# Kernel tuning notes

Measured on AMD Instinct MI355X. Metric: run time of the kernel, lower is better.

The kernel has to match this reference:

```python
import jax, jax.numpy as jnp
import numpy as np

G = 16          # graphs per side
NPG = 512       # nodes per graph
NSIDE = G * NPG # 8192 nodes per side
N = 2 * NSIDE   # 16384 nodes in combined batched graph
EPG = 4096      # edges per graph
E = 2 * G * EPG # 131072 edges
IN = 64; HID = 64; NH = 8; NC = 3
ALPHA = 0.2; EPS = 1e-5


def setup_inputs() -> dict:
    key = jax.random.key(0)
    ks = jax.random.split(key, 20)
    s = 0.05
    off = jnp.repeat(jnp.arange(2 * G, dtype=jnp.int32) * NPG, EPG)
    return {
        'nbd1': jax.random.normal(ks[0], (NSIDE, IN), jnp.float32),
        'nbd2': jax.random.normal(ks[1], (NSIDE, IN), jnp.float32),
        'ebd': jax.random.normal(ks[2], (E, IN), jnp.float32),
        'src': jax.random.randint(ks[3], (E,), 0, NPG, jnp.int32) + off,
        'dst': jax.random.randint(ks[4], (E,), 0, NPG, jnp.int32) + off,
        'node_gid': jnp.repeat(jnp.arange(2 * G, dtype=jnp.int32), NPG),
        'projW': jax.random.normal(ks[5], (4 * IN, HID), jnp.float32) * s,
        'W1': jax.random.normal(ks[6], (IN, NH * HID), jnp.float32) * s,
        'al1': jax.random.normal(ks[7], (NH, HID), jnp.float32) * s,
        'ar1': jax.random.normal(ks[8], (NH, HID), jnp.float32) * s,
        'ae1': jax.random.normal(ks[9], (NH, HID), jnp.float32) * s,
        'W2': jax.random.normal(ks[10], (NH * HID, NH * HID), jnp.float32) * s,
        'al2': jax.random.normal(ks[11], (NH, HID), jnp.float32) * s,
        'ar2': jax.random.normal(ks[12], (NH, HID), jnp.float32) * s,
        'ae2': jax.random.normal(ks[13], (NH, HID), jnp.float32) * s,
        'bn1_g': jnp.ones((2 * NH * HID,), jnp.float32),
        'bn1_b': jnp.zeros((2 * NH * HID,), jnp.float32),
        'fc1_W': jax.random.normal(ks[14], (2 * NH * HID, HID), jnp.float32) * s,
        'fc1_b': jnp.zeros((HID,), jnp.float32),
        'bn2_g': jnp.ones((HID,), jnp.float32),
        'bn2_b': jnp.zeros((HID,), jnp.float32),
        'fc2_W': jax.random.normal(ks[15], (HID, NC), jnp.float32) * s,
        'fc2_b': jnp.zeros((NC,), jnp.float32),
    }


def _segment_softmax(s, seg, n):
    # s: [E, H]; softmax over edges sharing the same destination node
    m = jax.ops.segment_max(s, seg, num_segments=n)
    ex = jnp.exp(s - m[seg])
    z = jax.ops.segment_sum(ex, seg, num_segments=n)
    return ex / jnp.maximum(z[seg], 1e-9)


def _gat_layer(hn, he, src, dst, n, W, al, ar, ae):
    nh, d = al.shape
    ft = (hn @ W).reshape(n, nh, d)            # [N,H,D]
    eft = (he @ W).reshape(-1, nh, d)          # [E,H,D]
    a1 = jnp.einsum('nhd,hd->nh', ft, al)
    a2 = jnp.einsum('nhd,hd->nh', ft, ar)
    a3 = jnp.einsum('ehd,hd->eh', eft, ae)
    a = a1[src] + a3 + a2[dst]                 # [E,H]
    a = jnp.where(a > 0, a, ALPHA * a)         # LeakyReLU(0.2)
    alpha = _segment_softmax(a, dst, n)[:, :, None]  # [E,H,1]
    f_cat = eft * alpha + ft[src] * alpha      # weighted edge + weighted src feat
    nft = jax.ops.segment_sum(f_cat, dst, num_segments=n)
    ret1 = jax.nn.elu(nft.reshape(n, nh * d))
    ret2 = jax.nn.elu(f_cat.reshape(f_cat.shape[0], nh * d))
    return ret1, ret2


def _bn(x, g, b):
    mu = jnp.mean(x, axis=0)
    v = jnp.var(x, axis=0)
    return (x - mu) * jax.lax.rsqrt(v + EPS) * g + b


def _forward(nbd1, nbd2, ebd, src, dst, node_gid, projW,
             W1, al1, ar1, ae1, W2, al2, ar2, ae2,
             bn1_g, bn1_b, fc1_W, fc1_b, bn2_g, bn2_b, fc2_W, fc2_b):
    # Node alignment (cross-graph soft attention, 2-D tensors as in source)
    att = nbd1 @ nbd2.T                                   # [N1,N2]
    x1a = jax.nn.softmax(att, axis=-1) @ nbd2
    x2a = jax.nn.softmax(att.T, axis=-1) @ nbd1
    q1 = jnp.concatenate([nbd1, x1a, nbd1 - x1a, nbd1 * x1a], axis=-1)
    q2 = jnp.concatenate([nbd2, x2a, nbd2 - x2a, nbd2 * x2a], axis=-1)
    h1 = jax.nn.relu(q1 @ projW)
    h2 = jax.nn.relu(q2 @ projW)
    h_n = jnp.concatenate([h1, h2], axis=0)               # [N,HID]
    h_e = ebd
    h_n, h_e = _gat_layer(h_n, h_e, src, dst, N, W1, al1, ar1, ae1)
    h_n, h_e = _gat_layer(h_n, h_e, src, dst, N, W2, al2, ar2, ae2)
    # dgl.mean_nodes
    cnt = jax.ops.segment_sum(jnp.ones((N,), h_n.dtype), node_gid, num_segments=2 * G)
    hg = jax.ops.segment_sum(h_n, node_gid, num_segments=2 * G) / cnt[:, None]
    x = jnp.concatenate([hg[:G], hg[G:2 * G]], axis=1)    # [G, 2*NH*HID]
    x = _bn(x, bn1_g, bn1_b)
    x = jax.nn.relu(x @ fc1_W + fc1_b)
    x = _bn(x, bn2_g, bn2_b)
    return x @ fc2_W + fc2_b                              # [G, NC]


def reference(nbd1, nbd2, ebd, src, dst, node_gid, projW,
              W1, al1, ar1, ae1, W2, al2, ar2, ae2,
              bn1_g, bn1_b, fc1_W, fc1_b, bn2_g, bn2_b, fc2_W, fc2_b):
    return _forward(nbd1, nbd2, ebd, src, dst, node_gid, projW,
                    W1, al1, ar1, ae1, W2, al2, ar2, ae2,
                    bn1_g, bn1_b, fc1_W, fc1_b, bn2_g, bn2_b, fc2_W, fc2_b)
```

## Files before the change

kernel.cpp:

```cpp
#include <hip/hip_runtime.h>


#define NSd 8192
#define NNd 16384
#define NEd 131072
#define KSPLIT 8

typedef unsigned short u16;
typedef unsigned int   u32;
typedef short bf16x8 __attribute__((ext_vector_type(8)));
typedef float f32x4  __attribute__((ext_vector_type(4)));
typedef float f32x16 __attribute__((ext_vector_type(16)));

__device__ __forceinline__ float bf2f(u16 u){ return __uint_as_float(((u32)u) << 16); }
__device__ __forceinline__ u16 f2bf(float f){
  u32 u = __float_as_uint(f);
  u += 0x7fffu + ((u >> 16) & 1u);
  return (u16)(u >> 16);
}
__device__ __forceinline__ u32 pkbf(float a, float b){
  u32 r;
  asm("v_cvt_pk_bf16_f32 %0, %1, %2" : "=v"(r) : "v"(a), "v"(b));
  return r;
}
__device__ __forceinline__ void pl32swap(u32& a, u32& b){
  auto r = __builtin_amdgcn_permlane32_swap(a, b, false, false);
  a = r[0]; b = r[1];
}
__device__ __forceinline__ float eluf(float x){ return x > 0.f ? x : expm1f(x); }
__device__ __forceinline__ float leaky(float x){ return x > 0.f ? x : 0.2f * x; }
__device__ __forceinline__ float ldin(const void* p, size_t i, int fl){
  return fl ? bf2f(((const u16*)p)[i]) : ((const float*)p)[i];
}
__device__ __forceinline__ void lse_merge(float& m, float& z, float om, float oz){
  float M = fmaxf(m, om);
  z = z * __expf(m - M) + oz * __expf(om - M);
  m = M;
}

static constexpr size_t OFF_WF   = 0;
static constexpr size_t OFF_CB   = 1529600;
static constexpr size_t OFF_U    = 1584896;
static constexpr size_t OFF_W1B  = 18362112;
static constexpr size_t OFF_W2B  = 18427648;
static constexpr size_t OFF_WE2B = 18951936;
static constexpr size_t OFF_AL1  = 35139328;
static constexpr size_t OFF_SA   = 39333632;
static constexpr size_t OFF_HNA  = 43527936;
static constexpr size_t OFF_DEG  = 77082368;
static constexpr size_t OFF_RP   = 77147904;
static constexpr size_t OFF_FILL = 77213696;
static constexpr size_t OFF_CIDX = 77279232;
static constexpr size_t OFF_RBIG = 77803520;
static constexpr size_t OFF_T    = 111357952;
static constexpr size_t OFF_XCAT = 144912384;
static constexpr size_t OFF_FLAG = 144977920;
static constexpr size_t WS_NEED  = 144978176;

static constexpr size_t T_X1A = 0;
static constexpr size_t T_X2A = 2097152;
static constexpr size_t T_HN0 = 4194304;
static constexpr size_t T_PZ  = 4194304;
static constexpr size_t T_AN1 = 8388608;
static constexpr size_t T_S   = 9437184;
static constexpr size_t T_Y   = 0;
static constexpr size_t T_G2  = 16777216;
static constexpr size_t T_Y1G = 0;
static constexpr size_t R_AN2 = 17301504;

static constexpr int WO_PROJ = 0,      WO_W1 = 16384;
static constexpr int WO_AL1 = 49152,   WO_AR1 = 49664,  WO_AE1 = 50176;
static constexpr int WO_W2  = 50688;
static constexpr int WO_AL2 = 312832,  WO_AR2 = 313344, WO_AE2 = 313856;
static constexpr int WO_B1G = 314368,  WO_B1B = 315392;
static constexpr int WO_F1W = 316416,  WO_F1B = 381952;
static constexpr int WO_B2G = 382016,  WO_B2B = 382080;
static constexpr int WO_F2W = 382144,  WO_F2B = 382336;
static constexpr int WO_END = 382339;

static constexpr int CB_WC1 = 0;
static constexpr int CB_WE1 = 1024;
static constexpr int CB_WC2 = 1536;
static constexpr int CB_WE2 = 9728;
static constexpr int CB_END = 13824;

__global__ __launch_bounds__(256) void detect_k(const u16* __restrict__ p, int* __restrict__ flag){
  __shared__ int bad;
  if (threadIdx.x == 0) bad = 0;
  __syncthreads();
  int b = 0;
  for (int i = threadIdx.x; i < 1024; i += 256){
    float f = bf2f(p[i]);
    if (!(fabsf(f) <= 100.f)) b++;
  }
  atomicAdd(&bad, b);
  __syncthreads();
  if (threadIdx.x == 0) *flag = (bad == 0) ? 1 : 0;
}

struct P17 { const void* p[17]; };

__global__ __launch_bounds__(256) void convw_k(P17 ps, float* __restrict__ wf, const int* __restrict__ flagp){
  const int i = blockIdx.x * 256 + threadIdx.x;
  if (i >= WO_END) return;
  const int fl = *flagp;
  const int ends[17] = {16384,49152,49664,50176,50688,312832,313344,313856,314368,
                        315392,316416,381952,382016,382080,382144,382336,382339};
  int seg = 0;
  while (i >= ends[seg]) seg++;
  const int start = seg ? ends[seg-1] : 0;
  wf[i] = ldin(ps.p[seg], i - start, fl);
}

__global__ __launch_bounds__(256) void convwT_k(const float* __restrict__ wf, u16* __restrict__ w1t,
                                                u16* __restrict__ w2t){
  const int i = blockIdx.x * 256 + threadIdx.x;
  if (i < 32768){
    const int c = i >> 6, k = i & 63;
    w1t[i] = f2bf(wf[WO_W1 + k * 512 + c]);
  } else if (i < 32768 + 262144){
    const int j = i - 32768;
    const int c = j >> 9, k = j & 511;
    w2t[j] = f2bf(wf[WO_W2 + k * 512 + c]);
  }
}

__global__ __launch_bounds__(256) void combos_k(const float* __restrict__ wf, float* __restrict__ cb,
                                                u16* __restrict__ we2b){
  const int i = blockIdx.x * 256 + threadIdx.x;
  if (i >= CB_END + 4096) return;
  if (i >= CB_END){ we2b[4096 + (i - CB_END)] = 0; return; }
  float acc = 0.f;
  if (i < 1024){
    const int o = i >> 6, d = i & 63, h = o & 7;
    const float* a = wf + ((o >> 3) ? WO_AR1 : WO_AL1) + h * 64;
    for (int dp = 0; dp < 64; dp++) acc += wf[WO_W1 + d * 512 + h * 64 + dp] * a[dp];
    cb[CB_WC1 + i] = acc;
  } else if (i < 1536){
    const int j = i - 1024, h = j >> 6, d = j & 63;
    for (int dp = 0; dp < 64; dp++) acc += wf[WO_W1 + d * 512 + h * 64 + dp] * wf[WO_AE1 + h * 64 + dp];
    cb[CB_WE1 + j] = acc;
  } else if (i < 9728){
    const int j = i - 1536, o = j >> 9, c = j & 511, h = o & 7;
    for (int dp = 0; dp < 64; dp++){
      const float av = (o >> 3) ? wf[WO_AR2 + h * 64 + dp]
                                : (wf[WO_AL2 + h * 64 + dp] - wf[WO_AE2 + h * 64 + dp]);
      acc += wf[WO_W2 + c * 512 + h * 64 + dp] * av;
    }
    cb[CB_WC2 + j] = acc;
  } else {
    const int j = i - 9728, h = j >> 9, c = j & 511;
    for (int dp = 0; dp < 64; dp++) acc += wf[WO_W2 + c * 512 + h * 64 + dp] * wf[WO_AE2 + h * 64 + dp];
    cb[CB_WE2 + j] = acc;
    we2b[j] = f2bf(acc);
  }
}

__global__ __launch_bounds__(256) void flash_mfma_k(const void* __restrict__ Qp, const void* __restrict__ Kp,
                                                    const int* __restrict__ flagp, float* __restrict__ pacc,
                                                    float* __restrict__ pz){
  const int fl = *flagp;
  __shared__ __align__(16) u16 Ks[2][32][64];
  __shared__ __align__(16) u16 Kt[2][64][40];
  const int t = threadIdx.x;
  const int w = t >> 6, l = t & 63;
  const int hi = l >> 5, ql = l & 31;
  const int q0 = blockIdx.x * 128;
  const int kbeg = blockIdx.y * 1024;
  const int sr = t & 31, scg = t >> 5;
  const int kp = t & 15, dq = t >> 4;

  bf16x8 bq[4];
  {
    const int qrow = q0 + w * 32 + ql;
    if (fl){
      const u16* qp = (const u16*)Qp + (size_t)qrow * 64 + hi * 8;
      #pragma unroll
      for (int s = 0; s < 4; s++) bq[s] = *(const bf16x8*)(qp + s * 16);
    } else {
      const float* qp = (const float*)Qp + (size_t)qrow * 64 + hi * 8;
      #pragma unroll
      for (int s = 0; s < 4; s++){
        union { u32 w_[4]; bf16x8 v; } u;
        #pragma unroll
        for (int i = 0; i < 4; i++) u.w_[i] = pkbf(qp[s*16 + 2*i], qp[s*16 + 2*i + 1]);
        bq[s] = u.v;
      }
    }
  }

  f32x16 accO0, accO1;
  #pragma unroll
  for (int i = 0; i < 16; i++){ accO0[i] = 0.f; accO1[i] = 0.f; }
  float lsum = 0.f;

  {
    const int kr = kbeg;
    if (fl){
      const u16* kb = (const u16*)Kp + (size_t)kr * 64;
      const uint4 s0 = *(const uint4*)(kb + (size_t)sr * 64 + scg * 8);
      const uint2 a0 = *(const uint2*)(kb + (size_t)(2*kp) * 64 + dq * 4);
      const uint2 b0 = *(const uint2*)(kb + (size_t)(2*kp + 1) * 64 + dq * 4);
      *(uint4*)((char*)&Ks[0][sr][0] + ((scg * 16) ^ ((sr & 7) << 4))) = s0;
      const u16* pa = (const u16*)&a0; const u16* pb = (const u16*)&b0;
      #pragma unroll
      for (int i = 0; i < 4; i++)
        *(u32*)&Kt[0][4*dq + i][2*kp] = (u32)pa[i] | ((u32)pb[i] << 16);
    } else {
      const float* kf = (const float*)Kp + (size_t)kr * 64;
      const float4 f0 = *(const float4*)(kf + (size_t)sr * 64 + scg * 8);
      const float4 f1 = *(const float4*)(kf + (size_t)sr * 64 + scg * 8 + 4);
      const float4 fa = *(const float4*)(kf + (size_t)(2*kp) * 64 + dq * 4);
      const float4 fb = *(const float4*)(kf + (size_t)(2*kp + 1) * 64 + dq * 4);
      union { u32 w_[4]; uint4 q; } uu;
      uu.w_[0] = pkbf(f0.x, f0.y); uu.w_[1] = pkbf(f0.z, f0.w);
      uu.w_[2] = pkbf(f1.x, f1.y); uu.w_[3] = pkbf(f1.z, f1.w);
      *(uint4*)((char*)&Ks[0][sr][0] + ((scg * 16) ^ ((sr & 7) << 4))) = uu.q;
      const float* faf = &fa.x; const float* fbf = &fb.x;
      #pragma unroll
      for (int i = 0; i < 4; i++)
        *(u32*)&Kt[0][4*dq + i][2*kp] = pkbf(faf[i], fbf[i]);
    }
  }

  for (int it = 0; it < 32; it++){
    const int cur = it & 1;
    __syncthreads();

    uint4 nKs; uint2 nKa, nKb;
    float4 nKsf0, nKsf1, nKaf, nKbf;
    const bool nx = (it + 1 < 32);
    if (nx){
      const int kr = kbeg + (it + 1) * 32;
      if (fl){
        const u16* kb = (const u16*)Kp + (size_t)kr * 64;
        nKs = *(const uint4*)(kb + (size_t)sr * 64 + scg * 8);
        nKa = *(const uint2*)(kb + (size_t)(2*kp) * 64 + dq * 4);
        nKb = *(const uint2*)(kb + (size_t)(2*kp + 1) * 64 + dq * 4);
      } else {
        const float* kf = (const float*)Kp + (size_t)kr * 64;
        nKsf0 = *(const float4*)(kf + (size_t)sr * 64 + scg * 8);
        nKsf1 = *(const float4*)(kf + (size_t)sr * 64 + scg * 8 + 4);
        nKaf  = *(const float4*)(kf + (size_t)(2*kp) * 64 + dq * 4);
        nKbf  = *(const float4*)(kf + (size_t)(2*kp + 1) * 64 + dq * 4);
      }
    }

    f32x16 accS;
    #pragma unroll
    for (int i = 0; i < 16; i++) accS[i] = 0.f;
    #pragma unroll
    for (int s = 0; s < 4; s++){
      const int byo = (s * 32 + hi * 16) ^ ((ql & 7) << 4);
      const bf16x8 a = *(const bf16x8*)((const char*)&Ks[cur][ql][0] + byo);
      accS = __builtin_amdgcn_mfma_f32_32x32x16_bf16(a, bq[s], accS, 0, 0, 0);
    }
    float p[16];
    #pragma unroll
    for (int r = 0; r < 16; r++) p[r] = exp2f(fmaf(accS[r], 1.44269504f, -46.1662413f));
    {
      const float s0 = (p[0] + p[1]) + (p[2] + p[3]);
      const float s1 = (p[4] + p[5]) + (p[6] + p[7]);
      const float s2 = (p[8] + p[9]) + (p[10] + p[11]);
      const float s3 = (p[12] + p[13]) + (p[14] + p[15]);
      lsum += (s0 + s1) + (s2 + s3);
    }
    u32 pk_[8];
    #pragma unroll
    for (int j = 0; j < 4; j++){
      pk_[2*j]     = pkbf(p[4*j],     p[4*j + 1]);
      pk_[2*j + 1] = pkbf(p[4*j + 2], p[4*j + 3]);
    }
    pl32swap(pk_[0], pk_[2]); pl32swap(pk_[1], pk_[3]);
    pl32swap(pk_[4], pk_[6]); pl32swap(pk_[5], pk_[7]);
    union { u32 w_[4]; bf16x8 v; } ua, ub;
    ua.w_[0] = pk_[0]; ua.w_[1] = pk_[1]; ua.w_[2] = pk_[2]; ua.w_[3] = pk_[3];
    ub.w_[0] = pk_[4]; ub.w_[1] = pk_[5]; ub.w_[2] = pk_[6]; ub.w_[3] = pk_[7];
    {
      const u16* kt0 = &Kt[cur][ql][hi * 8];
      accO0 = __builtin_amdgcn_mfma_f32_32x32x16_bf16(ua.v, *(const bf16x8*)kt0, accO0, 0, 0, 0);
      accO0 = __builtin_amdgcn_mfma_f32_32x32x16_bf16(ub.v, *(const bf16x8*)(kt0 + 16), accO0, 0, 0, 0);
      const u16* kt1 = &Kt[cur][32 + ql][hi * 8];
      accO1 = __builtin_amdgcn_mfma_f32_32x32x16_bf16(ua.v, *(const bf16x8*)kt1, accO1, 0, 0, 0);
      accO1 = __builtin_amdgcn_mfma_f32_32x32x16_bf16(ub.v, *(const bf16x8*)(kt1 + 16), accO1, 0, 0, 0);
    }

    if (nx){
      char* kd = (char*)&Ks[cur ^ 1][sr][0];
      const int byo = (scg * 16) ^ ((sr & 7) << 4);
      if (fl){
        *(uint4*)(kd + byo) = nKs;
        const u16* pa = (const u16*)&nKa; const u16* pb = (const u16*)&nKb;
        #pragma unroll
        for (int i = 0; i < 4; i++)
          *(u32*)&Kt[cur ^ 1][4*dq + i][2*kp] = (u32)pa[i] | ((u32)pb[i] << 16);
      } else {
        union { u32 w_[4]; uint4 q; } uu;
        uu.w_[0] = pkbf(nKsf0.x, nKsf0.y); uu.w_[1] = pkbf(nKsf0.z, nKsf0.w);
        uu.w_[2] = pkbf(nKsf1.x, nKsf1.y); uu.w_[3] = pkbf(nKsf1.z, nKsf1.w);
        *(uint4*)(kd + byo) = uu.q;
        const float* faf = &nKaf.x; const float* fbf = &nKbf.x;
        #pragma unroll
        for (int i = 0; i < 4; i++)
          *(u32*)&Kt[cur ^ 1][4*dq + i][2*kp] = pkbf(faf[i], fbf[i]);
      }
    }
  }

  const float zq = lsum + __shfl_xor(lsum, 32);
  const int rowb = q0 + w * 32;
  #pragma unroll
  for (int r = 0; r < 16; r++){
    const int m = (r & 3) + 8 * (r >> 2) + 4 * hi;
    float* pr = pacc + ((size_t)blockIdx.y * NSd + rowb + m) * 64;
    pr[ql]      = accO0[r];
    pr[32 + ql] = accO1[r];
  }
  if (hi == 0) pz[blockIdx.y * NSd + rowb + ql] = zq;
}

__global__ __launch_bounds__(256) void flash_merge_k(const float* __restrict__ pacc,
                                                     const float* __restrict__ pz, float* __restrict__ outp){
  const int t = threadIdx.x;
  const int r = blockIdx.x * 4 + (t >> 6);
  const int d = t & 63;
  float Zt = 0.f, v = 0.f;
  #pragma unroll
  for (int s = 0; s < KSPLIT; s++){
    Zt += pz[s * NSd + r];
    v  += pacc[((size_t)s * NSd + r) * 64 + d];
  }
  outp[(size_t)r * 64 + d] = v / Zt;
}

__global__ __launch_bounds__(256) void proj_k(const void* __restrict__ nbd1, const void* __restrict__ nbd2,
                                              const float* __restrict__ x1a, const float* __restrict__ x2a,
                                              const float* __restrict__ wf, float* __restrict__ hn0,
                                              const int* __restrict__ flagp){
  const int fl = *flagp;
  __shared__ float At[64][65], Bt[64][65];
  const int t = threadIdx.x, tx = t & 15, ty = t >> 4;
  const int m0 = blockIdx.x * 64;
  float acc[4][4] = {{0.f}};
  for (int kt = 0; kt < 256; kt += 64){
    __syncthreads();
    {
      const int i = t >> 2, c0 = (t & 3) * 16;
      const int mrow = m0 + i;
      const int side = mrow < NSd;
      const int mr = side ? mrow : mrow - NSd;
      const void* nb = side ? nbd1 : nbd2;
      const float* xa = side ? x1a : x2a;
      const int seg = kt >> 6;
      for (int c = 0; c < 16; c++){
        const int kk = c0 + c;
        const float nv = ldin(nb, (size_t)mr * 64 + kk, fl);
        const float av = xa[(size_t)mr * 64 + kk];
        At[i][kk] = (seg == 0) ? nv : (seg == 1) ? av : (seg == 2) ? (nv - av) : (nv * av);
      }
      const int kk = t >> 2;
      for (int c = 0; c < 16; c++) Bt[kk][c0 + c] = wf[WO_PROJ + (kt + kk) * 64 + c0 + c];
    }
    __syncthreads();
    #pragma unroll
    for (int k = 0; k < 64; k++){
      float a0 = At[ty*4+0][k], a1 = At[ty*4+1][k], a2 = At[ty*4+2][k], a3 = At[ty*4+3][k];
      float b0 = Bt[k][tx*4+0], b1 = Bt[k][tx*4+1], b2 = Bt[k][tx*4+2], b3 = Bt[k][tx*4+3];
      acc[0][0] = fmaf(a0,b0,acc[0][0]); acc[0][1] = fmaf(a0,b1,acc[0][1]); acc[0][2] = fmaf(a0,b2,acc[0][2]); acc[0][3] = fmaf(a0,b3,acc[0][3]);
      acc[1][0] = fmaf(a1,b0,acc[1][0]); acc[1][1] = fmaf(a1,b1,acc[1][1]); acc[1][2] = fmaf(a1,b2,acc[1][2]); acc[1][3] = fmaf(a1,b3,acc[1][3]);
      acc[2][0] = fmaf(a2,b0,acc[2][0]); acc[2][1] = fmaf(a2,b1,acc[2][1]); acc[2][2] = fmaf(a2,b2,acc[2][2]); acc[2][3] = fmaf(a2,b3,acc[2][3]);
      acc[3][0] = fmaf(a3,b0,acc[3][0]); acc[3][1] = fmaf(a3,b1,acc[3][1]); acc[3][2] = fmaf(a3,b2,acc[3][2]); acc[3][3] = fmaf(a3,b3,acc[3][3]);
    }
  }
  #pragma unroll
  for (int i = 0; i < 4; i++)
    #pragma unroll
    for (int j = 0; j < 4; j++)
      hn0[(size_t)(m0 + ty*4 + i) * 64 + tx*4 + j] = fmaxf(acc[i][j], 0.f);
}

__global__ __launch_bounds__(256) void an64_k(const float* __restrict__ hn0, const float* __restrict__ wc,
                                              float* __restrict__ an){
  const int id = blockIdx.x * 256 + threadIdx.x;
  const int n = id >> 4, o = id & 15;
  const float* row = hn0 + (size_t)n * 64;
  const float* wp = wc + o * 64;
  float acc = 0.f;
  for (int k = 0; k < 64; k += 4){
    const float4 r4 = *(const float4*)(row + k);
    const float4 w4 = *(const float4*)(wp + k);
    acc += r4.x*w4.x + r4.y*w4.y + r4.z*w4.z + r4.w*w4.w;
  }
  an[id] = acc;
}

__global__ __launch_bounds__(256) void anw_k(const float* __restrict__ HNA, const float* __restrict__ wc,
                                             float* __restrict__ an){
  __shared__ float W[16][516];
  const int t = threadIdx.x;
  for (int i = t; i < 8192; i += 256) W[i >> 9][i & 511] = wc[i];
  __syncthreads();
  const int node = blockIdx.x * 64 + (t >> 2);
  const int cb0 = (t & 3) * 4;
  const float* row = HNA + (size_t)node * 512;
  float acc[4] = {0.f, 0.f, 0.f, 0.f};
  for (int k = 0; k < 512; k += 4){
    const float4 r = *(const float4*)(row + k);
    #pragma unroll
    for (int j = 0; j < 4; j++){
      const float* wr = &W[cb0 + j][k];
      acc[j] += r.x * wr[0] + r.y * wr[1] + r.z * wr[2] + r.w * wr[3];
    }
  }
  #pragma unroll
  for (int j = 0; j < 4; j++) an[node * 16 + cb0 + j] = acc[j];
}

__global__ __launch_bounds__(256) void us1_k(const void* __restrict__ ebd, const float* __restrict__ hn0,
                                             const int* __restrict__ src, const int* __restrict__ dst,
                                             const float* __restrict__ cb, const float* __restrict__ an,
                                             const int* __restrict__ epos,
                                             u16* __restrict__ Ub, float* __restrict__ S,
                                             const int* __restrict__ flagp){
  __shared__ float we[512];
  const int t = threadIdx.x;
  for (int i = t; i < 512; i += 256) we[i] = cb[CB_WE1 + i];
  __syncthreads();
  const int fl = *flagp;
  const int id = blockIdx.x * 256 + t;
  const int e = id >> 4, q = id & 15, d0 = q * 4;
  const int sn = src[e];
  float ev[4];
  if (fl){
    const uint2 u = *(const uint2*)((const u16*)ebd + (size_t)e * 64 + d0);
    ev[0] = bf2f((u16)(u.x & 0xffffu)); ev[1] = bf2f((u16)(u.x >> 16));
    ev[2] = bf2f((u16)(u.y & 0xffffu)); ev[3] = bf2f((u16)(u.y >> 16));
  } else {
    const float4 f = *(const float4*)((const float*)ebd + (size_t)e * 64 + d0);
    ev[0] = f.x; ev[1] = f.y; ev[2] = f.z; ev[3] = f.w;
  }
  const float4 hv = *(const float4*)(hn0 + (size_t)sn * 64 + d0);
  ushort4 o;
  o.x = f2bf(ev[0] + hv.x); o.y = f2bf(ev[1] + hv.y);
  o.z = f2bf(ev[2] + hv.z); o.w = f2bf(ev[3] + hv.w);
  *(ushort4*)(Ub + (size_t)e * 64 + d0) = o;
  float p[8];
  #pragma unroll
  for (int h = 0; h < 8; h++){
    const float* wp = we + h * 64 + d0;
    p[h] = ev[0]*wp[0] + ev[1]*wp[1] + ev[2]*wp[2] + ev[3]*wp[3];
  }
  #pragma unroll
  for (int h = 0; h < 8; h++){
    p[h] += __shfl_xor(p[h], 1); p[h] += __shfl_xor(p[h], 2);
    p[h] += __shfl_xor(p[h], 4); p[h] += __shfl_xor(p[h], 8);
  }
  if (q == 0){
    const int dn = dst[e];
    const size_t pos = epos[e];
    #pragma unroll
    for (int h = 0; h < 8; h++)
      S[pos * 8 + h] = leaky(an[sn * 16 + h] + p[h] + an[dn * 16 + 8 + h]);
  }
}

__global__ __launch_bounds__(256) void segalpha_pos_k(const float* __restrict__ S, const int* __restrict__ rp,
                                                      float* __restrict__ AL){
  const int node = blockIdx.x * 4 + (threadIdx.x >> 6);
  const int l = threadIdx.x & 63;
  const int h = l & 7, i0 = l >> 3;
  const int beg = rp[node], end = rp[node + 1];
  float m = -1e30f, z = 0.f;
  for (int base = beg; base < end; base += 8){
    const int idx = base + i0;
    float v = -1e30f, cc = 0.f;
    if (idx < end){ v = S[(size_t)idx * 8 + h]; cc = 1.f; }
    lse_merge(m, z, v, cc);
  }
  #pragma unroll
  for (int off = 8; off < 64; off <<= 1){
    float om = __shfl_xor(m, off), oz = __shfl_xor(z, off);
    lse_merge(m, z, om, oz);
  }
  const float rz = 1.f / fmaxf(z, 1e-9f);
  for (int base = beg; base < end; base += 8){
    const int idx = base + i0;
    if (idx < end)
      AL[(size_t)idx * 8 + h] = __expf(S[(size_t)idx * 8 + h] - m) * rz;
  }
}

__global__ __launch_bounds__(256) void g1b_k(const float* __restrict__ AL, const u16* __restrict__ Ub,
                                             const int* __restrict__ rp, const int* __restrict__ cidx,
                                             u16* __restrict__ G1b){
  const int n = blockIdx.x;
  const int t = threadIdx.x;
  const int d = t & 63, hh = t >> 6;
  const int beg = rp[n], end = rp[n + 1];
  float a0 = 0.f, a1 = 0.f;
  for (int idx = beg; idx < end; idx++){
    const int e = cidx[idx];
    const float uv = bf2f(Ub[(size_t)e * 64 + d]);
    a0 = fmaf(AL[(size_t)idx * 8 + hh],     uv, a0);
    a1 = fmaf(AL[(size_t)idx * 8 + hh + 4], uv, a1);
  }
  G1b[(size_t)(n * 8 + hh)     * 64 + d] = f2bf(a0);
  G1b[(size_t)(n * 8 + hh + 4) * 64 + d] = f2bf(a1);
}

__global__ __launch_bounds__(256) void nft1m_k(const u16* __restrict__ G1b, const u16* __restrict__ W1T,
                                               float* __restrict__ HNA){
  const int t = threadIdx.x;
  const int w = t >> 6, lane = t & 63;
  const int col = lane & 15, quad = lane >> 4;
  const int h = blockIdx.y;
  const int nl0 = blockIdx.x * 32;
  const int mt = (w & 1) * 16;
  const int nb = (w >> 1) * 2;
  const u16* arow = G1b + ((size_t)(nl0 + mt + col) * 8 + h) * 64;
  const bf16x8 a0 = *(const bf16x8*)(arow + quad*8);
  const bf16x8 a1 = *(const bf16x8*)(arow + 32 + quad*8);
  #pragma unroll
  for (int nn = 0; nn < 2; nn++){
    const int nt = nb + nn;
    const u16* brow = W1T + (size_t)(h*64 + nt*16 + col) * 64;
    const bf16x8 b0 = *(const bf16x8*)(brow + quad*8);
    const bf16x8 b1 = *(const bf16x8*)(brow + 32 + quad*8);
    f32x4 acc = (f32x4){0.f, 0.f, 0.f, 0.f};
    acc = __builtin_amdgcn_mfma_f32_16x16x32_bf16(a0, b0, acc, 0, 0, 0);
    acc = __builtin_amdgcn_mfma_f32_16x16x32_bf16(a1, b1, acc, 0, 0, 0);
    #pragma unroll
    for (int i = 0; i < 4; i++)
      HNA[(size_t)(nl0 + mt + quad*4 + i) * 512 + h*64 + nt*16 + col] = eluf(acc[i]);
  }
}

__global__ __launch_bounds__(256) void y3_k(const u16* __restrict__ Ub, const float* __restrict__ AL1,
                                            const float* __restrict__ HNA, const u16* __restrict__ W1T,
                                            const int* __restrict__ src, const int* __restrict__ cidx,
                                            u16* __restrict__ Y, const int s){
  __shared__ __align__(16) u16 Us[32][72];
  __shared__ float als[256];
  __shared__ int Es[32], Ss[32];
  const int t = threadIdx.x;
  const int w = t >> 6, lane = t & 63;
  const int col = lane & 15, quad = lane >> 4;
  const int mw = (w & 1) * 16;
  const int hw = (w >> 1) * 4;
  const int ep0 = s * 16384 + blockIdx.x * 32;
  if (t < 32){ const int e = cidx[ep0 + t]; Es[t] = e; Ss[t] = src[e]; }
  als[t] = AL1[(size_t)ep0 * 8 + t];
  __syncthreads();
  {
    const int r = t >> 3, seg = (t & 7) * 8;
    *(ushort4*)&Us[r][seg]     = *(const ushort4*)(Ub + (size_t)Es[r] * 64 + seg);
    *(ushort4*)&Us[r][seg + 4] = *(const ushort4*)(Ub + (size_t)Es[r] * 64 + seg + 4);
  }
  __syncthreads();
  const bf16x8 a0 = *(const bf16x8*)&Us[mw + col][quad*8];
  const bf16x8 a1 = *(const bf16x8*)&Us[mw + col][32 + quad*8];
  #pragma unroll
  for (int hh = 0; hh < 4; hh++){
    const int h = hw + hh;
    #pragma unroll
    for (int nt = 0; nt < 4; nt++){
      const u16* brow = W1T + (size_t)(h*64 + nt*16 + col) * 64;
      const bf16x8 b0 = *(const bf16x8*)(brow + quad*8);
      const bf16x8 b1 = *(const bf16x8*)(brow + 32 + quad*8);
      f32x4 acc = (f32x4){0.f, 0.f, 0.f, 0.f};
      acc = __builtin_amdgcn_mfma_f32_16x16x32_bf16(a0, b0, acc, 0, 0, 0);
      acc = __builtin_amdgcn_mfma_f32_16x16x32_bf16(a1, b1, acc, 0, 0, 0);
      #pragma unroll
      for (int i = 0; i < 4; i++){
        const int er = mw + quad*4 + i;
        const float v = eluf(als[er*8 + h] * acc[i]) + HNA[(size_t)Ss[er] * 512 + h*64 + nt*16 + col];
        Y[(size_t)(blockIdx.x*32 + er) * 512 + h*64 + nt*16 + col] = f2bf(v);
      }
    }
  }
}

__global__ __launch_bounds__(256) void score2_k(const u16* __restrict__ Y, const u16* __restrict__ we2b,
                                                const float* __restrict__ AN2, const int* __restrict__ src,
                                                const int* __restrict__ dst, const int* __restrict__ cidx,
                                                float* __restrict__ SA, const int s){
  __shared__ int Se[64], De[64];
  const int t = threadIdx.x;
  const int w = t >> 6, lane = t & 63;
  const int col = lane & 15, quad = lane >> 4;
  const int p0 = blockIdx.x * 64;
  const int base = s * 16384;
  if (t < 64){ const int e = cidx[base + p0 + t]; Se[t] = src[e]; De[t] = dst[e]; }
  __syncthreads();
  const u16* arow = Y + (size_t)(p0 + w*16 + col) * 512;
  const u16* brow = we2b + (size_t)col * 512;
  f32x4 acc = (f32x4){0.f, 0.f, 0.f, 0.f};
  #pragma unroll
  for (int ks = 0; ks < 16; ks++){
    const bf16x8 a = *(const bf16x8*)(arow + ks*32 + quad*8);
    const bf16x8 b = *(const bf16x8*)(brow + ks*32 + quad*8);
    acc = __builtin_amdgcn_mfma_f32_16x16x32_bf16(a, b, acc, 0, 0, 0);
  }
  if (col < 8){
    #pragma unroll
    for (int i = 0; i < 4; i++){
      const int rl = w*16 + quad*4 + i;
      const size_t pos = base + p0 + rl;
      SA[pos * 8 + col] = leaky(AN2[Se[rl]*16 + col] + acc[i] + AN2[De[rl]*16 + 8 + col]);
    }
  }
}

__global__ __launch_bounds__(256) void sg2_k(const u16* __restrict__ Y, const int* __restrict__ rp,
                                             const float* __restrict__ SA, u16* __restrict__ G2,
                                             const int s){
  __shared__ float sc[64][8];
  __shared__ float mh[8], rzh[8];
  const int t = threadIdx.x;
  const int nl = blockIdx.x;
  const int n = s * 2048 + nl;
  const int beg = rp[n], end = rp[n + 1], m = end - beg;
  const int base = s * 16384;
  const bool small = (m <= 64);
  {
    const int h = t >> 5, l32 = t & 31;
    float mm = -1e30f, zz = 0.f;
    for (int i = l32; i < m; i += 32)
      lse_merge(mm, zz, SA[(size_t)(beg + i) * 8 + h], 1.f);
    #pragma unroll
    for (int off = 1; off < 32; off <<= 1){
      const float om = __shfl_xor(mm, off), oz = __shfl_xor(zz, off);
      lse_merge(mm, zz, om, oz);
    }
    if (l32 == 0){ mh[h] = mm; rzh[h] = 1.f / fmaxf(zz, 1e-9f); }
  }
  __syncthreads();
  if (small){
    for (int idx = t; idx < m * 8; idx += 256){
      const int i = idx >> 3, h = idx & 7;
      sc[i][h] = __expf(SA[(size_t)(beg + i) * 8 + h] - mh[h]) * rzh[h];
    }
  }
  __syncthreads();
  {
    const int d0 = t * 2;
    float ac[8][2] = {{0.f}};
    for (int i = 0; i < m; i++){
      const int epl = beg + i - base;
      const u32 yv = *(const u32*)(Y + (size_t)epl * 512 + d0);
      const float y0 = bf2f((u16)(yv & 0xffffu)), y1 = bf2f((u16)(yv >> 16));
      float al[8];
      if (small){
        #pragma unroll
        for (int h = 0; h < 8; h++) al[h] = sc[i][h];
      } else {
        #pragma unroll
        for (int h = 0; h < 8; h++)
          al[h] = __expf(SA[(size_t)(beg + i) * 8 + h] - mh[h]) * rzh[h];
      }
      #pragma unroll
      for (int h = 0; h < 8; h++){
        ac[h][0] = fmaf(al[h], y0, ac[h][0]);
        ac[h][1] = fmaf(al[h], y1, ac[h][1]);
      }
    }
    #pragma unroll
    for (int h = 0; h < 8; h++){
      const u32 o = (u32)f2bf(ac[h][0]) | ((u32)f2bf(ac[h][1]) << 16);
      *(u32*)(G2 + ((size_t)nl * 8 + h) * 512 + d0) = o;
    }
  }
}

__global__ __launch_bounds__(256) void nft2m_k(const u16* __restrict__ G2, const u16* __restrict__ W2T,
                                               u16* __restrict__ HNB, const int s){
  const int t = threadIdx.x;
  const int w = t >> 6, lane = t & 63;
  const int col = lane & 15, quad = lane >> 4;
  const int h = blockIdx.y;
  const int nl0 = blockIdx.x * 32;
  const int mt = (w & 1) * 16;
  const int nb = (w >> 1) * 2;
  const u16* arow = G2 + ((size_t)((nl0 + mt + col) * 8) + h) * 512;
  #pragma unroll
  for (int nn = 0; nn < 2; nn++){
    const int nt = nb + nn;
    const u16* brow = W2T + (size_t)(h*64 + nt*16 + col) * 512;
    f32x4 acc = (f32x4){0.f, 0.f, 0.f, 0.f};
    #pragma unroll
    for (int ks = 0; ks < 16; ks++){
      const bf16x8 a = *(const bf16x8*)(arow + ks*32 + quad*8);
      const bf16x8 b = *(const bf16x8*)(brow + ks*32 + quad*8);
      acc = __builtin_amdgcn_mfma_f32_16x16x32_bf16(a, b, acc, 0, 0, 0);
    }
    #pragma unroll
    for (int i = 0; i < 4; i++)
      HNB[(size_t)(s*2048 + nl0 + mt + quad*4 + i) * 512 + h*64 + nt*16 + col] = f2bf(eluf(acc[i]));
  }
}

__global__ __launch_bounds__(256) void hist_k(const int* __restrict__ dst, int* __restrict__ deg){
  const int e = blockIdx.x * 256 + threadIdx.x;
  if (e < NEd) atomicAdd(&deg[dst[e]], 1);
}
__global__ __launch_bounds__(256) void scan_k(const int* __restrict__ deg, int* __restrict__ rp,
                                              int* __restrict__ fill){
  __shared__ int wsum[4];
  const int t = threadIdx.x;
  const int lane = t & 63, wid = t >> 6;
  const int base = t * 64;
  int s = 0;
  for (int i = 0; i < 64; i++) s += deg[base + i];
  int v = s;
  #pragma unroll
  for (int off = 1; off < 64; off <<= 1){
    const int u = __shfl_up(v, off);
    if (lane >= off) v += u;
  }
  if (lane == 63) wsum[wid] = v;
  __syncthreads();
  int add = 0;
  #pragma unroll
  for (int wq = 0; wq < 4; wq++) if (wq < wid) add += wsum[wq];
  int off0 = add + v - s;
  for (int i = 0; i < 64; i++){
    rp[base + i] = off0; fill[base + i] = off0;
    off0 += deg[base + i];
  }
  if (t == 255) rp[NNd] = off0;
}
__global__ __launch_bounds__(256) void scatter_k(const int* __restrict__ dst, int* __restrict__ fill,
                                                 int* __restrict__ cidx, int* __restrict__ epos){
  const int e = blockIdx.x * 256 + threadIdx.x;
  if (e < NEd){
    int pos = atomicAdd(&fill[dst[e]], 1);
    cidx[pos] = e;
    epos[e] = pos;
  }
}

__global__ __launch_bounds__(256) void mean_k(const u16* __restrict__ HNB, float* __restrict__ xcat){
  const int sg = blockIdx.x;
  const int t = threadIdx.x;
  const int g = (sg < 16) ? sg : sg - 16;
  const int half = (sg < 16) ? 0 : 1;
  const int c0 = t * 2;
  float s0 = 0.f, s1 = 0.f;
  const u16* base = HNB + (size_t)sg * 512 * 512;
  for (int n = 0; n < 512; n++){
    const u32 u = *(const u32*)(base + (size_t)n * 512 + c0);
    s0 += bf2f((u16)(u & 0xffffu));
    s1 += bf2f((u16)(u >> 16));
  }
  xcat[g * 1024 + half * 512 + c0]     = s0 * (1.f / 512.f);
  xcat[g * 1024 + half * 512 + c0 + 1] = s1 * (1.f / 512.f);
}

__global__ __launch_bounds__(256) void bn1_k(float* __restrict__ xcat, const float* __restrict__ wf){
  const int j = blockIdx.x * 256 + threadIdx.x;
  float mu = 0.f;
  #pragma unroll
  for (int g = 0; g < 16; g++) mu += xcat[g * 1024 + j];
  mu *= (1.f / 16.f);
  float var = 0.f;
  #pragma unroll
  for (int g = 0; g < 16; g++){ const float d = xcat[g * 1024 + j] - mu; var += d * d; }
  var *= (1.f / 16.f);
  const float sc = rsqrtf(var + 1e-5f) * wf[WO_B1G + j];
  const float sh = wf[WO_B1B + j] - mu * sc;
  #pragma unroll
  for (int g = 0; g < 16; g++) xcat[g * 1024 + j] = xcat[g * 1024 + j] * sc + sh;
}

__global__ __launch_bounds__(256) void fc1_k(const float* __restrict__ xcat, const float* __restrict__ wf,
                                             float* __restrict__ y1g){
  __shared__ float xs[1024];
  __shared__ float ps[4][64];
  const int t = threadIdx.x, g = blockIdx.x;
  for (int i = t; i < 1024; i += 256) xs[i] = xcat[g * 1024 + i];
  __syncthreads();
  const int c = t & 63, kq = t >> 6;
  float acc = 0.f;
  #pragma unroll 4
  for (int k = kq * 256; k < kq * 256 + 256; k++)
    acc = fmaf(xs[k], wf[WO_F1W + k * 64 + c], acc);
  ps[kq][c] = acc;
  __syncthreads();
  if (t < 64){
    const float a = ps[0][t] + ps[1][t] + ps[2][t] + ps[3][t] + wf[WO_F1B + t];
    y1g[g * 64 + t] = fmaxf(a, 0.f);
  }
}

__global__ __launch_bounds__(256) void head2_k(const float* __restrict__ y1g, const float* __restrict__ wf,
                                               void* __restrict__ outp, const int* __restrict__ flagp){
  __shared__ float y1s[16][64];
  __shared__ float mu2s[64], sc2s[64];
  const int t = threadIdx.x;
  for (int i = t; i < 1024; i += 256) y1s[i >> 6][i & 63] = y1g[i];
  __syncthreads();
  if (t < 64){
    float mu = 0.f;
    #pragma unroll
    for (int g = 0; g < 16; g++) mu += y1s[g][t];
    mu *= (1.f / 16.f);
    float var = 0.f;
    #pragma unroll
    for (int g = 0; g < 16; g++){ const float d = y1s[g][t] - mu; var += d * d; }
    var *= (1.f / 16.f);
    mu2s[t] = mu; sc2s[t] = rsqrtf(var + 1e-5f) * wf[WO_B2G + t];
  }
  __syncthreads();
  if (t < 48){
    const int gg = t / 3, c = t % 3;
    float acc = wf[WO_F2B + c];
    #pragma unroll
    for (int k = 0; k < 64; k++){
      const float y2 = (y1s[gg][k] - mu2s[k]) * sc2s[k] + wf[WO_B2B + k];
      acc = fmaf(y2, wf[WO_F2W + k * 3 + c], acc);
    }
    if (*flagp) ((u16*)outp)[t] = f2bf(acc);
    else        ((float*)outp)[t] = acc;
  }
}

extern "C" void kernel_launch(void* const* d_in, const int* in_sizes, int n_in,
                              void* d_out, int out_size, void* d_ws, size_t ws_size,
                              hipStream_t stream) {
  (void)in_sizes; (void)n_in; (void)out_size;
  if (ws_size < WS_NEED) return;

  const int* src = (const int*)d_in[3];
  const int* dst = (const int*)d_in[4];
  char* w = (char*)d_ws;

  float* wf   = (float*)(w + OFF_WF);
  float* cb   = (float*)(w + OFF_CB);
  u16*   Ub   = (u16*)(w + OFF_U);
  u16*   W1T  = (u16*)(w + OFF_W1B);
  u16*   W2T  = (u16*)(w + OFF_W2B);
  u16*   we2b = (u16*)(w + OFF_WE2B);
  float* AL1  = (float*)(w + OFF_AL1);
  float* SA   = (float*)(w + OFF_SA);
  int*   epos = (int*)(w + OFF_SA);
  float* HNA  = (float*)(w + OFF_HNA);
  int*   deg  = (int*)(w + OFF_DEG);
  int*   rp   = (int*)(w + OFF_RP);
  int*   fill = (int*)(w + OFF_FILL);
  int*   cidx = (int*)(w + OFF_CIDX);
  float* rbig = (float*)(w + OFF_RBIG);
  float* xcat = (float*)(w + OFF_XCAT);
  int*   flag = (int*)(w + OFF_FLAG);

  float* x1a  = (float*)(w + OFF_T + T_X1A);
  float* x2a  = (float*)(w + OFF_T + T_X2A);
  float* hn0  = (float*)(w + OFF_T + T_HN0);
  float* AN1  = (float*)(w + OFF_T + T_AN1);
  float* S    = (float*)(w + OFF_T + T_S);
  u16*   Y    = (u16*)(w + OFF_T + T_Y);
  u16*   G2   = (u16*)(w + OFF_T + T_G2);
  float* y1g  = (float*)(w + OFF_T + T_Y1G);

  float* pacc = rbig;
  float* pz   = (float*)(w + OFF_T + T_PZ);
  u16*   G1b  = (u16*)(w + OFF_RBIG);
  u16*   HNB  = (u16*)(w + OFF_RBIG);
  float* AN2  = (float*)(w + OFF_RBIG + R_AN2);

  detect_k<<<1, 256, 0, stream>>>((const u16*)d_in[0], flag);
  P17 ps;
  for (int i = 0; i < 17; i++) ps.p[i] = d_in[6 + i];
  convw_k<<<(WO_END + 255) / 256, 256, 0, stream>>>(ps, wf, flag);
  convwT_k<<<(32768 + 262144 + 255) / 256, 256, 0, stream>>>(wf, W1T, W2T);
  combos_k<<<(CB_END + 4096 + 255) / 256, 256, 0, stream>>>(wf, cb, we2b);

  hipMemsetAsync(deg, 0, NNd * sizeof(int), stream);
  hist_k<<<NEd / 256, 256, 0, stream>>>(dst, deg);
  scan_k<<<1, 256, 0, stream>>>(deg, rp, fill);
  scatter_k<<<NEd / 256, 256, 0, stream>>>(dst, fill, cidx, epos);

  flash_mfma_k<<<dim3(64, KSPLIT), 256, 0, stream>>>(d_in[0], d_in[1], flag, pacc, pz);
  flash_merge_k<<<NSd / 4, 256, 0, stream>>>(pacc, pz, x1a);
  flash_mfma_k<<<dim3(64, KSPLIT), 256, 0, stream>>>(d_in[1], d_in[0], flag, pacc, pz);
  flash_merge_k<<<NSd / 4, 256, 0, stream>>>(pacc, pz, x2a);

  proj_k<<<NNd / 64, 256, 0, stream>>>(d_in[0], d_in[1], x1a, x2a, wf, hn0, flag);

  an64_k<<<NNd * 16 / 256, 256, 0, stream>>>(hn0, cb + CB_WC1, AN1);
  us1_k<<<NEd * 16 / 256, 256, 0, stream>>>(d_in[2], hn0, src, dst, cb, AN1, epos, Ub, S, flag);
  segalpha_pos_k<<<NNd / 4, 256, 0, stream>>>(S, rp, AL1);
  g1b_k<<<NNd, 256, 0, stream>>>(AL1, Ub, rp, cidx, G1b);
  nft1m_k<<<dim3(NNd / 32, 8), 256, 0, stream>>>(G1b, W1T, HNA);

  anw_k<<<NNd / 64, 256, 0, stream>>>(HNA, cb + CB_WC2, AN2);

  for (int s = 0; s < 8; s++){
    y3_k<<<512, 256, 0, stream>>>(Ub, AL1, HNA, W1T, src, cidx, Y, s);
    score2_k<<<256, 256, 0, stream>>>(Y, we2b, AN2, src, dst, cidx, SA, s);
    sg2_k<<<2048, 256, 0, stream>>>(Y, rp, SA, G2, s);
    nft2m_k<<<dim3(64, 8), 256, 0, stream>>>(G2, W2T, HNB, s);
  }

  mean_k<<<32, 256, 0, stream>>>(HNB, xcat);
  bn1_k<<<4, 256, 0, stream>>>(xcat, wf);
  fc1_k<<<16, 256, 0, stream>>>(xcat, wf, y1g);
  head2_k<<<1, 256, 0, stream>>>(y1g, wf, d_out, flag);
}
```

Measured before the change: 925.5 us.

## Split layer-1 edge scores into MFMA kernel, widen layer-2 chunks, parallelize mean

The layer-1 edge score projection moves out of us1_k into a new score1_k. That kernel walks edges in CSR order and computes the ebd·We1 dot products with bf16 MFMA, which removes the epos scatter array and the per-edge shuffle reductions. The layer-2 loop now runs y3/score2 over 4 chunks of 32768 edges instead of 8 of 16384, while sg2/nft2m still run per 2048-node slice. G2 moves to a different workspace region so the larger Y buffer has room. mean_k is split across 256 blocks that combine their partial sums with atomic adds into a zeroed xcat, at the cost of an extra memset and bf16 rounding of ebd in the score.

```diff
diff --git a/kernel.cpp b/kernel.cpp
--- a/kernel.cpp
+++ b/kernel.cpp
@@ -44,6 +44,7 @@
 static constexpr size_t OFF_W1B  = 18362112;
 static constexpr size_t OFF_W2B  = 18427648;
 static constexpr size_t OFF_WE2B = 18951936;
+static constexpr size_t OFF_WE1B = 18968320;
 static constexpr size_t OFF_AL1  = 35139328;
 static constexpr size_t OFF_SA   = 39333632;
 static constexpr size_t OFF_HNA  = 43527936;
@@ -64,9 +65,9 @@
 static constexpr size_t T_AN1 = 8388608;
 static constexpr size_t T_S   = 9437184;
 static constexpr size_t T_Y   = 0;
-static constexpr size_t T_G2  = 16777216;
 static constexpr size_t T_Y1G = 0;
 static constexpr size_t R_AN2 = 17301504;
+static constexpr size_t R_G2  = 18350080;
 
 static constexpr int WO_PROJ = 0,      WO_W1 = 16384;
 static constexpr int WO_AL1 = 49152,   WO_AR1 = 49664,  WO_AE1 = 50176;
@@ -126,9 +127,10 @@
 }
 
 __global__ __launch_bounds__(256) void combos_k(const float* __restrict__ wf, float* __restrict__ cb,
-                                                u16* __restrict__ we2b){
+                                                u16* __restrict__ we2b, u16* __restrict__ we1b){
   const int i = blockIdx.x * 256 + threadIdx.x;
-  if (i >= CB_END + 4096) return;
+  if (i >= CB_END + 4096 + 512) return;
+  if (i >= CB_END + 4096){ we1b[512 + (i - CB_END - 4096)] = 0; return; }
   if (i >= CB_END){ we2b[4096 + (i - CB_END)] = 0; return; }
   float acc = 0.f;
   if (i < 1024){
@@ -140,6 +142,7 @@
     const int j = i - 1024, h = j >> 6, d = j & 63;
     for (int dp = 0; dp < 64; dp++) acc += wf[WO_W1 + d * 512 + h * 64 + dp] * wf[WO_AE1 + h * 64 + dp];
     cb[CB_WE1 + j] = acc;
+    we1b[j] = f2bf(acc);
   } else if (i < 9728){
     const int j = i - 1536, o = j >> 9, c = j & 511, h = o & 7;
     for (int dp = 0; dp < 64; dp++){
@@ -417,17 +420,10 @@
 }
 
 __global__ __launch_bounds__(256) void us1_k(const void* __restrict__ ebd, const float* __restrict__ hn0,
-                                             const int* __restrict__ src, const int* __restrict__ dst,
-                                             const float* __restrict__ cb, const float* __restrict__ an,
-                                             const int* __restrict__ epos,
-                                             u16* __restrict__ Ub, float* __restrict__ S,
+                                             const int* __restrict__ src, u16* __restrict__ Ub,
                                              const int* __restrict__ flagp){
-  __shared__ float we[512];
-  const int t = threadIdx.x;
-  for (int i = t; i < 512; i += 256) we[i] = cb[CB_WE1 + i];
-  __syncthreads();
   const int fl = *flagp;
-  const int id = blockIdx.x * 256 + t;
+  const int id = blockIdx.x * 256 + threadIdx.x;
   const int e = id >> 4, q = id & 15, d0 = q * 4;
   const int sn = src[e];
   float ev[4];
@@ -444,23 +440,48 @@
   o.x = f2bf(ev[0] + hv.x); o.y = f2bf(ev[1] + hv.y);
   o.z = f2bf(ev[2] + hv.z); o.w = f2bf(ev[3] + hv.w);
   *(ushort4*)(Ub + (size_t)e * 64 + d0) = o;
-  float p[8];
-  #pragma unroll
-  for (int h = 0; h < 8; h++){
-    const float* wp = we + h * 64 + d0;
-    p[h] = ev[0]*wp[0] + ev[1]*wp[1] + ev[2]*wp[2] + ev[3]*wp[3];
-  }
-  #pragma unroll
-  for (int h = 0; h < 8; h++){
-    p[h] += __shfl_xor(p[h], 1); p[h] += __shfl_xor(p[h], 2);
-    p[h] += __shfl_xor(p[h], 4); p[h] += __shfl_xor(p[h], 8);
-  }
-  if (q == 0){
-    const int dn = dst[e];
-    const size_t pos = epos[e];
-    #pragma unroll
-    for (int h = 0; h < 8; h++)
-      S[pos * 8 + h] = leaky(an[sn * 16 + h] + p[h] + an[dn * 16 + 8 + h]);
+}
+
+__global__ __launch_bounds__(256) void score1_k(const void* __restrict__ ebd, const u16* __restrict__ we1b,
+                                                const float* __restrict__ an, const int* __restrict__ src,
+                                                const int* __restrict__ dst, const int* __restrict__ cidx,
+                                                float* __restrict__ S, const int* __restrict__ flagp){
+  __shared__ int Se[64], De[64], Ee[64];
+  const int t = threadIdx.x;
+  const int w = t >> 6, lane = t & 63;
+  const int col = lane & 15, quad = lane >> 4;
+  const int p0 = blockIdx.x * 64;
+  if (t < 64){ const int e = cidx[p0 + t]; Ee[t] = e; Se[t] = src[e]; De[t] = dst[e]; }
+  __syncthreads();
+  const int fl = *flagp;
+  const int ea = Ee[w*16 + col];
+  bf16x8 a0, a1;
+  if (fl){
+    const u16* ap = (const u16*)ebd + (size_t)ea * 64;
+    a0 = *(const bf16x8*)(ap + quad*8);
+    a1 = *(const bf16x8*)(ap + 32 + quad*8);
+  } else {
+    const float* ap = (const float*)ebd + (size_t)ea * 64;
+    union { u32 w_[4]; bf16x8 v; } u0, u1;
+    #pragma unroll
+    for (int i = 0; i < 4; i++){
+      u0.w_[i] = pkbf(ap[quad*8 + 2*i],      ap[quad*8 + 2*i + 1]);
+      u1.w_[i] = pkbf(ap[32 + quad*8 + 2*i], ap[32 + quad*8 + 2*i + 1]);
+    }
+    a0 = u0.v; a1 = u1.v;
+  }
+  const u16* brow = we1b + (size_t)col * 64;
+  const bf16x8 b0 = *(const bf16x8*)(brow + quad*8);
+  const bf16x8 b1 = *(const bf16x8*)(brow + 32 + quad*8);
+  f32x4 acc = (f32x4){0.f, 0.f, 0.f, 0.f};
+  acc = __builtin_amdgcn_mfma_f32_16x16x32_bf16(a0, b0, acc, 0, 0, 0);
+  acc = __builtin_amdgcn_mfma_f32_16x16x32_bf16(a1, b1, acc, 0, 0, 0);
+  if (col < 8){
+    #pragma unroll
+    for (int i = 0; i < 4; i++){
+      const int rl = w*16 + quad*4 + i;
+      S[(size_t)(p0 + rl) * 8 + col] = leaky(an[Se[rl]*16 + col] + acc[i] + an[De[rl]*16 + 8 + col]);
+    }
   }
 }
 
@@ -538,7 +559,7 @@
 __global__ __launch_bounds__(256) void y3_k(const u16* __restrict__ Ub, const float* __restrict__ AL1,
                                             const float* __restrict__ HNA, const u16* __restrict__ W1T,
                                             const int* __restrict__ src, const int* __restrict__ cidx,
-                                            u16* __restrict__ Y, const int s){
+                                            u16* __restrict__ Y, const int s2){
   __shared__ __align__(16) u16 Us[32][72];
   __shared__ float als[256];
   __shared__ int Es[32], Ss[32];
@@ -547,7 +568,7 @@
   const int col = lane & 15, quad = lane >> 4;
   const int mw = (w & 1) * 16;
   const int hw = (w >> 1) * 4;
-  const int ep0 = s * 16384 + blockIdx.x * 32;
+  const int ep0 = s2 * 32768 + blockIdx.x * 32;
   if (t < 32){ const int e = cidx[ep0 + t]; Es[t] = e; Ss[t] = src[e]; }
   als[t] = AL1[(size_t)ep0 * 8 + t];
   __syncthreads();
@@ -583,14 +604,14 @@
 __global__ __launch_bounds__(256) void score2_k(const u16* __restrict__ Y, const u16* __restrict__ we2b,
                                                 const float* __restrict__ AN2, const int* __restrict__ src,
                                                 const int* __restrict__ dst, const int* __restrict__ cidx,
-                                                float* __restrict__ SA, const int s){
+                                                float* __restrict__ SA, const int s2){
   __shared__ int Se[64], De[64];
   const int t = threadIdx.x;
   const int w = t >> 6, lane = t & 63;
   const int col = lane & 15, quad = lane >> 4;
   const int p0 = blockIdx.x * 64;
-  const int base = s * 16384;
-  if (t < 64){ const int e = cidx[base + p0 + t]; Se[t] = src[e]; De[t] = dst[e]; }
+  const int gbase = s2 * 32768;
+  if (t < 64){ const int e = cidx[gbase + p0 + t]; Se[t] = src[e]; De[t] = dst[e]; }
   __syncthreads();
   const u16* arow = Y + (size_t)(p0 + w*16 + col) * 512;
   const u16* brow = we2b + (size_t)col * 512;
@@ -605,7 +626,7 @@
     #pragma unroll
     for (int i = 0; i < 4; i++){
       const int rl = w*16 + quad*4 + i;
-      const size_t pos = base + p0 + rl;
+      const size_t pos = gbase + p0 + rl;
       SA[pos * 8 + col] = leaky(AN2[Se[rl]*16 + col] + acc[i] + AN2[De[rl]*16 + 8 + col]);
     }
   }
@@ -620,7 +641,7 @@
   const int nl = blockIdx.x;
   const int n = s * 2048 + nl;
   const int beg = rp[n], end = rp[n + 1], m = end - beg;
-  const int base = s * 16384;
+  const int base = (s >> 1) * 32768;
   const bool small = (m <= 64);
   {
     const int h = t >> 5, l32 = t & 31;
@@ -730,30 +751,29 @@
   if (t == 255) rp[NNd] = off0;
 }
 __global__ __launch_bounds__(256) void scatter_k(const int* __restrict__ dst, int* __restrict__ fill,
-                                                 int* __restrict__ cidx, int* __restrict__ epos){
+                                                 int* __restrict__ cidx){
   const int e = blockIdx.x * 256 + threadIdx.x;
   if (e < NEd){
     int pos = atomicAdd(&fill[dst[e]], 1);
     cidx[pos] = e;
-    epos[e] = pos;
   }
 }
 
 __global__ __launch_bounds__(256) void mean_k(const u16* __restrict__ HNB, float* __restrict__ xcat){
-  const int sg = blockIdx.x;
+  const int sg = blockIdx.x >> 3, chunk = blockIdx.x & 7;
   const int t = threadIdx.x;
   const int g = (sg < 16) ? sg : sg - 16;
   const int half = (sg < 16) ? 0 : 1;
   const int c0 = t * 2;
   float s0 = 0.f, s1 = 0.f;
-  const u16* base = HNB + (size_t)sg * 512 * 512;
-  for (int n = 0; n < 512; n++){
+  const u16* base = HNB + ((size_t)sg * 512 + chunk * 64) * 512;
+  for (int n = 0; n < 64; n++){
     const u32 u = *(const u32*)(base + (size_t)n * 512 + c0);
     s0 += bf2f((u16)(u & 0xffffu));
     s1 += bf2f((u16)(u >> 16));
   }
-  xcat[g * 1024 + half * 512 + c0]     = s0 * (1.f / 512.f);
-  xcat[g * 1024 + half * 512 + c0 + 1] = s1 * (1.f / 512.f);
+  atomicAdd(&xcat[g * 1024 + half * 512 + c0],     s0 * (1.f / 512.f));
+  atomicAdd(&xcat[g * 1024 + half * 512 + c0 + 1], s1 * (1.f / 512.f));
 }
 
 __global__ __launch_bounds__(256) void bn1_k(float* __restrict__ xcat, const float* __restrict__ wf){
@@ -840,9 +860,9 @@
   u16*   W1T  = (u16*)(w + OFF_W1B);
   u16*   W2T  = (u16*)(w + OFF_W2B);
   u16*   we2b = (u16*)(w + OFF_WE2B);
+  u16*   we1b = (u16*)(w + OFF_WE1B);
   float* AL1  = (float*)(w + OFF_AL1);
   float* SA   = (float*)(w + OFF_SA);
-  int*   epos = (int*)(w + OFF_SA);
   float* HNA  = (float*)(w + OFF_HNA);
   int*   deg  = (int*)(w + OFF_DEG);
   int*   rp   = (int*)(w + OFF_RP);
@@ -858,7 +878,6 @@
   float* AN1  = (float*)(w + OFF_T + T_AN1);
   float* S    = (float*)(w + OFF_T + T_S);
   u16*   Y    = (u16*)(w + OFF_T + T_Y);
-  u16*   G2   = (u16*)(w + OFF_T + T_G2);
   float* y1g  = (float*)(w + OFF_T + T_Y1G);
 
   float* pacc = rbig;
@@ -866,18 +885,19 @@
   u16*   G1b  = (u16*)(w + OFF_RBIG);
   u16*   HNB  = (u16*)(w + OFF_RBIG);
   float* AN2  = (float*)(w + OFF_RBIG + R_AN2);
+  u16*   G2   = (u16*)(w + OFF_RBIG + R_G2);
 
   detect_k<<<1, 256, 0, stream>>>((const u16*)d_in[0], flag);
   P17 ps;
   for (int i = 0; i < 17; i++) ps.p[i] = d_in[6 + i];
   convw_k<<<(WO_END + 255) / 256, 256, 0, stream>>>(ps, wf, flag);
   convwT_k<<<(32768 + 262144 + 255) / 256, 256, 0, stream>>>(wf, W1T, W2T);
-  combos_k<<<(CB_END + 4096 + 255) / 256, 256, 0, stream>>>(wf, cb, we2b);
+  combos_k<<<(CB_END + 4096 + 512 + 255) / 256, 256, 0, stream>>>(wf, cb, we2b, we1b);
 
   hipMemsetAsync(deg, 0, NNd * sizeof(int), stream);
   hist_k<<<NEd / 256, 256, 0, stream>>>(dst, deg);
   scan_k<<<1, 256, 0, stream>>>(deg, rp, fill);
-  scatter_k<<<NEd / 256, 256, 0, stream>>>(dst, fill, cidx, epos);
+  scatter_k<<<NEd / 256, 256, 0, stream>>>(dst, fill, cidx);
 
   flash_mfma_k<<<dim3(64, KSPLIT), 256, 0, stream>>>(d_in[0], d_in[1], flag, pacc, pz);
   flash_merge_k<<<NSd / 4, 256, 0, stream>>>(pacc, pz, x1a);
@@ -887,21 +907,26 @@
   proj_k<<<NNd / 64, 256, 0, stream>>>(d_in[0], d_in[1], x1a, x2a, wf, hn0, flag);
 
   an64_k<<<NNd * 16 / 256, 256, 0, stream>>>(hn0, cb + CB_WC1, AN1);
-  us1_k<<<NEd * 16 / 256, 256, 0, stream>>>(d_in[2], hn0, src, dst, cb, AN1, epos, Ub, S, flag);
+  us1_k<<<NEd * 16 / 256, 256, 0, stream>>>(d_in[2], hn0, src, Ub, flag);
+  score1_k<<<NEd / 64, 256, 0, stream>>>(d_in[2], we1b, AN1, src, dst, cidx, S, flag);
   segalpha_pos_k<<<NNd / 4, 256, 0, stream>>>(S, rp, AL1);
   g1b_k<<<NNd, 256, 0, stream>>>(AL1, Ub, rp, cidx, G1b);
   nft1m_k<<<dim3(NNd / 32, 8), 256, 0, stream>>>(G1b, W1T, HNA);
 
   anw_k<<<NNd / 64, 256, 0, stream>>>(HNA, cb + CB_WC2, AN2);
 
-  for (int s = 0; s < 8; s++){
-    y3_k<<<512, 256, 0, stream>>>(Ub, AL1, HNA, W1T, src, cidx, Y, s);
-    score2_k<<<256, 256, 0, stream>>>(Y, we2b, AN2, src, dst, cidx, SA, s);
-    sg2_k<<<2048, 256, 0, stream>>>(Y, rp, SA, G2, s);
-    nft2m_k<<<dim3(64, 8), 256, 0, stream>>>(G2, W2T, HNB, s);
-  }
-
-  mean_k<<<32, 256, 0, stream>>>(HNB, xcat);
+  for (int s2 = 0; s2 < 4; s2++){
+    y3_k<<<1024, 256, 0, stream>>>(Ub, AL1, HNA, W1T, src, cidx, Y, s2);
+    score2_k<<<512, 256, 0, stream>>>(Y, we2b, AN2, src, dst, cidx, SA, s2);
+    for (int sub = 0; sub < 2; sub++){
+      const int s = s2 * 2 + sub;
+      sg2_k<<<2048, 256, 0, stream>>>(Y, rp, SA, G2, s);
+      nft2m_k<<<dim3(64, 8), 256, 0, stream>>>(G2, W2T, HNB, s);
+    }
+  }
+
+  hipMemsetAsync(xcat, 0, 16 * 1024 * sizeof(float), stream);
+  mean_k<<<256, 256, 0, stream>>>(HNB, xcat);
   bn1_k<<<4, 256, 0, stream>>>(xcat, wf);
   fc1_k<<<16, 256, 0, stream>>>(xcat, wf, y1g);
   head2_k<<<1, 256, 0, stream>>>(y1g, wf, d_out, flag);
```

After: 819.9 us. 11.4% less time.
